# Optimization experiments

Hardware: AMD Instinct MI355X
Metric: run time of the kernel (lower is better)

## Reference

```python
import jax, jax.numpy as jnp
import numpy as np

N_NODES = 50000


def _gcn_conv(h, src, dst, W, b):
    # h: [N, d_in] -> [N, d_out]; symmetric-normalized aggregation with self-loops
    N = h.shape[0]
    h = h @ W  # transform first (d_out < d_in), like PyG GCNConv
    deg = jax.ops.segment_sum(jnp.ones_like(dst, dtype=h.dtype), dst, num_segments=N)
    dinv = jnp.where(deg > 0, jax.lax.rsqrt(jnp.maximum(deg, 1.0)), 0.0)
    norm = dinv[src] * dinv[dst]  # [E']
    msg = h[src] * norm[:, None]  # [E', d_out]
    out = jax.ops.segment_sum(msg, dst, num_segments=N)
    return out + b


def setup_inputs() -> dict:
    key = jax.random.key(0)
    k1, k2, k3, k4 = jax.random.split(key, 4)
    dim_in, dim_h, dim_out, E = 512, 96, 40, 800000
    x = jax.random.normal(k1, (N_NODES, dim_in), dtype=jnp.float32)
    edge_index = jax.random.randint(k2, (2, E), 0, N_NODES, dtype=jnp.int64)
    W1 = jax.random.normal(k3, (dim_in, dim_h), dtype=jnp.float32) / np.sqrt(dim_in)
    b1 = jnp.zeros((dim_h,), dtype=jnp.float32)
    W2 = jax.random.normal(k4, (dim_h, dim_out), dtype=jnp.float32) / np.sqrt(dim_h)
    b2 = jnp.zeros((dim_out,), dtype=jnp.float32)
    return {"x": x, "edge_index": edge_index, "W1": W1, "b1": b1, "W2": W2, "b2": b2}


def reference(x, edge_index, W1, b1, W2, b2):
    N = x.shape[0]
    loops = jnp.arange(N, dtype=edge_index.dtype)
    src = jnp.concatenate([edge_index[0], loops])
    dst = jnp.concatenate([edge_index[1], loops])
    h = jax.nn.relu(_gcn_conv(x, src, dst, W1, b1))
    # dropout p=0.5 is identity in eval mode (training=False)
    logits = _gcn_conv(h, src, dst, W2, b2)
    return (logits, jax.nn.log_softmax(logits, axis=1))
```

## Files before the change

### kernel.cpp

```cpp
#include <hip/hip_runtime.h>
#include <hip/hip_bf16.h>
#include <cstdint>
#include <cstddef>

#define DIN 512
#define DH  96
#define DOUT 40

typedef __attribute__((ext_vector_type(8))) short s8v;
typedef __attribute__((ext_vector_type(4))) float f4v;

__device__ __forceinline__ ushort f2bf(float f) {
    uint u = __float_as_uint(f);
    u += 0x7fffu + ((u >> 16) & 1u);
    return (ushort)(u >> 16);
}
__device__ __forceinline__ uint f2bf2(float lo, float hi) {
    __hip_bfloat162 h = __float22bfloat162_rn(make_float2(lo, hi));
    return *(uint*)&h;
}
__device__ __forceinline__ float bflo(uint u) { return __uint_as_float(u << 16); }
__device__ __forceinline__ float bfhi(uint u) { return __uint_as_float(u & 0xffff0000u); }

__global__ __launch_bounds__(256) void k_prep(
    const float* __restrict__ W1, const float* __restrict__ W2,
    int* __restrict__ cnt, ushort* __restrict__ W1T, ushort* __restrict__ W2T, int N)
{
    int i = blockIdx.x * 256 + threadIdx.x;
    if (i < N) cnt[i] = 0;
    if (i < DIN * DH) {
        int k = i / DH, n = i % DH;
        W1T[(size_t)n * DIN + k] = f2bf(W1[i]);
    }
    if (i < 48 * DH) {
        int n = i / DH, k = i % DH;
        W2T[i] = (n < DOUT) ? f2bf(W2[(size_t)k * DOUT + n]) : (ushort)0;
    }
}

__global__ __launch_bounds__(256) void k_hist(
    const int* __restrict__ dst, int* __restrict__ cnt, int* __restrict__ pos, int E)
{
    int e = blockIdx.x * 256 + threadIdx.x;
    if (e < E) pos[e] = atomicAdd(&cnt[dst[e]], 1);
}

__global__ __launch_bounds__(256) void k_blocksum(const int* __restrict__ cnt, int* __restrict__ bsum, int N) {
    int i = blockIdx.x * 256 + threadIdx.x;
    int c = (i < N) ? cnt[i] : 0;
    #pragma unroll
    for (int off = 32; off >= 1; off >>= 1) c += __shfl_down(c, off, 64);
    __shared__ int wsum[4];
    if ((threadIdx.x & 63) == 0) wsum[threadIdx.x >> 6] = c;
    __syncthreads();
    if (threadIdx.x == 0) bsum[blockIdx.x] = wsum[0] + wsum[1] + wsum[2] + wsum[3];
}

__global__ __launch_bounds__(256) void k_scan_small(const int* __restrict__ bsum, int* __restrict__ boff, int SB) {
    __shared__ int p[256];
    int tid = threadIdx.x;
    int v = (tid < SB) ? bsum[tid] : 0;
    p[tid] = v;
    __syncthreads();
    #pragma unroll
    for (int off = 1; off < 256; off <<= 1) {
        int t = (tid >= off) ? p[tid - off] : 0;
        __syncthreads();
        p[tid] += t;
        __syncthreads();
    }
    if (tid < SB) boff[tid] = p[tid] - v;
}

__global__ __launch_bounds__(256) void k_rowptr(
    const int* __restrict__ cnt, const int* __restrict__ boff,
    int* __restrict__ row_ptr, float* __restrict__ dinv, int N)
{
    __shared__ int p[256];
    int tid = threadIdx.x;
    int i = blockIdx.x * 256 + tid;
    int c = (i < N) ? cnt[i] : 0;
    p[tid] = c;
    __syncthreads();
    #pragma unroll
    for (int off = 1; off < 256; off <<= 1) {
        int t = (tid >= off) ? p[tid - off] : 0;
        __syncthreads();
        p[tid] += t;
        __syncthreads();
    }
    int excl = p[tid] - c;
    if (i < N) {
        int base = boff[blockIdx.x] + excl;
        row_ptr[i] = base;
        dinv[i] = rsqrtf(1.0f + (float)c);
        if (i == N - 1) row_ptr[N] = base + c;
    }
}

__global__ __launch_bounds__(256) void k_fill(
    const int* __restrict__ src, const int* __restrict__ dst,
    const int* __restrict__ row_ptr, const int* __restrict__ pos,
    int* __restrict__ adj, int E)
{
    int e = blockIdx.x * 256 + threadIdx.x;
    if (e >= E) return;
    adj[row_ptr[dst[e]] + pos[e]] = src[e];
}

__global__ __launch_bounds__(256) void k_gemm1(
    const float* __restrict__ x, const ushort* __restrict__ W1T,
    const float* __restrict__ dinv, ushort* __restrict__ hs1, int N)
{
    __shared__ __align__(16) ushort lds[28672];
    const int tid = threadIdx.x;
    const int row0 = blockIdx.x * 128;
    const int lane = tid & 63, w = tid >> 6;
    const int rb = (w >> 1) * 64, cb = (w & 1) * 48;
    const int lm = lane & 15, lq = lane >> 4;

    int aof[4][2], bof[3][2];
    #pragma unroll
    for (int i = 0; i < 4; ++i)
        #pragma unroll
        for (int ks = 0; ks < 2; ++ks) {
            int r = rb + i * 16 + lm, c = ks * 32 + lq * 8;
            aof[i][ks] = r * 64 + (c ^ ((r & 7) << 3));
        }
    #pragma unroll
    for (int j = 0; j < 3; ++j)
        #pragma unroll
        for (int ks = 0; ks < 2; ++ks) {
            int n = cb + j * 16 + lm, c = ks * 32 + lq * 8;
            bof[j][ks] = 16384 + n * 64 + (c ^ ((n & 7) << 3));
        }

    f4v acc[4][3];
    #pragma unroll
    for (int i = 0; i < 4; ++i)
        #pragma unroll
        for (int j = 0; j < 3; ++j) acc[i][j] = (f4v)0.f;

    const int sr = tid >> 1, scb = (tid & 1) * 32;

    auto stage = [&](int kt, int buf) {
        int k0 = kt * 64;
        int gr = row0 + sr;
        ushort* A = lds + buf * 8192;
        #pragma unroll
        for (int s = 0; s < 4; ++s) {
            int c = scb + s * 8;
            float4 v0 = make_float4(0.f, 0.f, 0.f, 0.f), v1 = v0;
            if (gr < N) {
                const float* pp = &x[(size_t)gr * DIN + k0 + c];
                v0 = *(const float4*)pp;
                v1 = *(const float4*)(pp + 4);
            }
            uint4 wv;
            wv.x = f2bf2(v0.x, v0.y);
            wv.y = f2bf2(v0.z, v0.w);
            wv.z = f2bf2(v1.x, v1.y);
            wv.w = f2bf2(v1.z, v1.w);
            *(uint4*)&A[sr * 64 + (c ^ ((sr & 7) << 3))] = wv;
        }
        ushort* B = lds + 16384 + buf * 6144;
        #pragma unroll
        for (int it = 0; it < 3; ++it) {
            int ss = tid + it * 256;
            int n = ss >> 3, c = (ss & 7) * 8;
            uint4 wv = *(const uint4*)&W1T[(size_t)n * DIN + k0 + c];
            *(uint4*)&B[n * 64 + (c ^ ((n & 7) << 3))] = wv;
        }
    };

    stage(0, 0);
    for (int kt = 0; kt < 8; ++kt) {
        __syncthreads();
        if (kt < 7) stage(kt + 1, (kt + 1) & 1);
        const int ab = (kt & 1) * 8192;
        const int bb = (kt & 1) * 6144;
        #pragma unroll
        for (int ks = 0; ks < 2; ++ks) {
            s8v b0 = *(s8v*)&lds[bof[0][ks] + bb];
            s8v b1 = *(s8v*)&lds[bof[1][ks] + bb];
            s8v b2 = *(s8v*)&lds[bof[2][ks] + bb];
            #pragma unroll
            for (int i = 0; i < 4; ++i) {
                s8v a = *(s8v*)&lds[aof[i][ks] + ab];
                acc[i][0] = __builtin_amdgcn_mfma_f32_16x16x32_bf16(a, b0, acc[i][0], 0, 0, 0);
                acc[i][1] = __builtin_amdgcn_mfma_f32_16x16x32_bf16(a, b1, acc[i][1], 0, 0, 0);
                acc[i][2] = __builtin_amdgcn_mfma_f32_16x16x32_bf16(a, b2, acc[i][2], 0, 0, 0);
            }
        }
    }

    #pragma unroll
    for (int i = 0; i < 4; ++i) {
        int gr0 = row0 + rb + i * 16 + lq * 4;
        #pragma unroll
        for (int q = 0; q < 4; ++q) {
            int gr = gr0 + q;
            if (gr < N) {
                float di = dinv[gr];
                #pragma unroll
                for (int j = 0; j < 3; ++j)
                    hs1[(size_t)gr * DH + cb + j * 16 + lm] = f2bf(acc[i][j][q] * di);
            }
        }
    }
}

__global__ __launch_bounds__(256) void k_agg1(
    const int* __restrict__ row_ptr, const int* __restrict__ adj,
    const float* __restrict__ dinv, const ushort* __restrict__ hs1,
    const float* __restrict__ b1, ushort* __restrict__ h1, int N)
{
    int t = blockIdx.x * 256 + threadIdx.x;
    int node = t >> 6, lane = t & 63;
    if (node >= N) return;
    int c = lane << 1;
    const bool act = (c < DH);

    float a0 = 0.f, a1 = 0.f;
    if (act) {
        uint u = *(const uint*)&hs1[(size_t)node * DH + c];
        a0 = bflo(u); a1 = bfhi(u);
    }
    int e = row_ptr[node], e1 = row_ptr[node + 1];
    for (; e + 7 < e1; e += 8) {
        int s0 = adj[e],     s1 = adj[e + 1], s2 = adj[e + 2], s3 = adj[e + 3];
        int s4 = adj[e + 4], s5 = adj[e + 5], s6 = adj[e + 6], s7 = adj[e + 7];
        if (act) {
            uint u0 = *(const uint*)&hs1[(size_t)s0 * DH + c];
            uint u1 = *(const uint*)&hs1[(size_t)s1 * DH + c];
            uint u2 = *(const uint*)&hs1[(size_t)s2 * DH + c];
            uint u3 = *(const uint*)&hs1[(size_t)s3 * DH + c];
            uint u4 = *(const uint*)&hs1[(size_t)s4 * DH + c];
            uint u5 = *(const uint*)&hs1[(size_t)s5 * DH + c];
            uint u6 = *(const uint*)&hs1[(size_t)s6 * DH + c];
            uint u7 = *(const uint*)&hs1[(size_t)s7 * DH + c];
            a0 += bflo(u0); a1 += bfhi(u0);
            a0 += bflo(u1); a1 += bfhi(u1);
            a0 += bflo(u2); a1 += bfhi(u2);
            a0 += bflo(u3); a1 += bfhi(u3);
            a0 += bflo(u4); a1 += bfhi(u4);
            a0 += bflo(u5); a1 += bfhi(u5);
            a0 += bflo(u6); a1 += bfhi(u6);
            a0 += bflo(u7); a1 += bfhi(u7);
        }
    }
    for (; e < e1; ++e) {
        int s = adj[e];
        if (act) {
            uint u = *(const uint*)&hs1[(size_t)s * DH + c];
            a0 += bflo(u); a1 += bfhi(u);
        }
    }
    if (act) {
        float di = dinv[node];
        float r0 = fmaxf(fmaf(a0, di, b1[c]), 0.f);
        float r1 = fmaxf(fmaf(a1, di, b1[c + 1]), 0.f);
        *(uint*)&h1[(size_t)node * DH + c] = f2bf2(r0, r1);
    }
}

__global__ __launch_bounds__(256) void k_gemm2(
    const ushort* __restrict__ h1, const ushort* __restrict__ W2T,
    const float* __restrict__ dinv, float* __restrict__ hs2, int N)
{
    __shared__ __align__(16) ushort lds[16384 + 48 * 128];
    const int tid = threadIdx.x;
    const int row0 = blockIdx.x * 128;

    for (int f = tid; f < 576; f += 256) {
        int r = f / 12, c = (f % 12) * 8;
        uint4 v = *(const uint4*)&W2T[r * DH + c];
        *(uint4*)&lds[16384 + r * 128 + (c ^ ((r & 7) << 3))] = v;
    }
    {
        int r = tid >> 1, half = tid & 1;
        int gr = row0 + r;
        #pragma unroll
        for (int i = 0; i < 6; ++i) {
            int c = half * 48 + i * 8;
            uint4 v = make_uint4(0, 0, 0, 0);
            if (gr < N) v = *(const uint4*)&h1[(size_t)gr * DH + c];
            *(uint4*)&lds[r * 128 + (c ^ ((r & 7) << 3))] = v;
        }
    }
    __syncthreads();

    const int lane = tid & 63, w = tid >> 6;
    const int rb = w * 32, lm = lane & 15, lq = lane >> 4;
    f4v acc[2][3];
    #pragma unroll
    for (int i = 0; i < 2; ++i)
        #pragma unroll
        for (int j = 0; j < 3; ++j) acc[i][j] = (f4v)0.f;

    #pragma unroll
    for (int ks = 0; ks < 3; ++ks) {
        int kk = ks * 32 + lq * 8;
        s8v b[3];
        #pragma unroll
        for (int j = 0; j < 3; ++j) {
            int n = j * 16 + lm;
            b[j] = *(s8v*)&lds[16384 + n * 128 + (kk ^ ((n & 7) << 3))];
        }
        #pragma unroll
        for (int i = 0; i < 2; ++i) {
            int r = rb + i * 16 + lm;
            s8v a = *(s8v*)&lds[r * 128 + (kk ^ ((r & 7) << 3))];
            #pragma unroll
            for (int j = 0; j < 3; ++j)
                acc[i][j] = __builtin_amdgcn_mfma_f32_16x16x32_bf16(a, b[j], acc[i][j], 0, 0, 0);
        }
    }

    #pragma unroll
    for (int i = 0; i < 2; ++i) {
        int gr0 = row0 + rb + i * 16 + lq * 4;
        #pragma unroll
        for (int q = 0; q < 4; ++q) {
            int gr = gr0 + q;
            if (gr < N) {
                float di = dinv[gr];
                #pragma unroll
                for (int j = 0; j < 3; ++j) {
                    int col = j * 16 + lm;
                    if (col < DOUT)
                        hs2[(size_t)gr * DOUT + col] = acc[i][j][q] * di;
                }
            }
        }
    }
}

__global__ __launch_bounds__(256) void k_agg2sm(
    const int* __restrict__ row_ptr, const int* __restrict__ adj,
    const float* __restrict__ dinv, const float* __restrict__ hs2,
    const float* __restrict__ b2, float* __restrict__ out,
    float* __restrict__ lsm, int N)
{
    int t = blockIdx.x * 256 + threadIdx.x;
    int node = t >> 6, lane = t & 63;
    if (node >= N) return;
    const bool act = lane < DOUT;

    float acc = act ? hs2[(size_t)node * DOUT + lane] : 0.f;
    int e = row_ptr[node], e1 = row_ptr[node + 1];
    for (; e + 7 < e1; e += 8) {
        int s0 = adj[e],     s1 = adj[e + 1], s2 = adj[e + 2], s3 = adj[e + 3];
        int s4 = adj[e + 4], s5 = adj[e + 5], s6 = adj[e + 6], s7 = adj[e + 7];
        if (act) {
            float v0 = hs2[(size_t)s0 * DOUT + lane];
            float v1 = hs2[(size_t)s1 * DOUT + lane];
            float v2 = hs2[(size_t)s2 * DOUT + lane];
            float v3 = hs2[(size_t)s3 * DOUT + lane];
            float v4 = hs2[(size_t)s4 * DOUT + lane];
            float v5 = hs2[(size_t)s5 * DOUT + lane];
            float v6 = hs2[(size_t)s6 * DOUT + lane];
            float v7 = hs2[(size_t)s7 * DOUT + lane];
            acc += ((v0 + v1) + (v2 + v3)) + ((v4 + v5) + (v6 + v7));
        }
    }
    for (; e < e1; ++e) {
        int s = adj[e];
        if (act) acc += hs2[(size_t)s * DOUT + lane];
    }

    float v = act ? fmaf(acc, dinv[node], b2[lane]) : -1e30f;
    float m = v;
    #pragma unroll
    for (int off = 32; off >= 1; off >>= 1) m = fmaxf(m, __shfl_xor(m, off));
    float ex = act ? __expf(v - m) : 0.f;
    float s = ex;
    #pragma unroll
    for (int off = 32; off >= 1; off >>= 1) s += __shfl_xor(s, off);
    float lse = m + __logf(s);
    if (act) {
        out[(size_t)node * DOUT + lane] = v;
        lsm[(size_t)node * DOUT + lane] = v - lse;
    }
}

extern "C" void kernel_launch(void* const* d_in, const int* in_sizes, int n_in,
                              void* d_out, int out_size, void* d_ws, size_t ws_size,
                              hipStream_t stream) {
    const float* x  = (const float*)d_in[0];
    const int*   ei = (const int*)d_in[1];
    const float* W1 = (const float*)d_in[2];
    const float* b1 = (const float*)d_in[3];
    const float* W2 = (const float*)d_in[4];
    const float* b2 = (const float*)d_in[5];

    const int N = in_sizes[0] / DIN;
    const int E = in_sizes[1] / 2;
    const int* srcp = ei;
    const int* dstp = ei + E;
    const int SB = (N + 255) / 256;

    ushort* hs1 = (ushort*)d_ws;
    ushort* h1  = hs1 + (size_t)N * DH;
    float* hs2  = (float*)(h1 + (size_t)N * DH);
    float* dinv = hs2 + (size_t)N * DOUT;
    ushort* W1T = (ushort*)(dinv + N);
    ushort* W2T = W1T + (size_t)DH * DIN;
    int* cnt     = (int*)(W2T + 48 * DH);
    int* row_ptr = cnt + N;
    int* adj     = row_ptr + N + 1;
    int* pos     = adj + E;
    int* bsum    = pos + E;
    int* boff    = bsum + SB;

    float* out = (float*)d_out;
    float* lsm = out + (size_t)N * DOUT;

    const int gE = (E + 255) / 256;

    k_prep<<<SB, 256, 0, stream>>>(W1, W2, cnt, W1T, W2T, N);
    k_hist<<<gE, 256, 0, stream>>>(dstp, cnt, pos, E);
    k_blocksum<<<SB, 256, 0, stream>>>(cnt, bsum, N);
    k_scan_small<<<1, 256, 0, stream>>>(bsum, boff, SB);
    k_rowptr<<<SB, 256, 0, stream>>>(cnt, boff, row_ptr, dinv, N);
    k_fill<<<gE, 256, 0, stream>>>(srcp, dstp, row_ptr, pos, adj, E);

    k_gemm1<<<(N + 127) / 128, 256, 0, stream>>>(x, W1T, dinv, hs1, N);
    k_agg1<<<(int)(((size_t)N * 64 + 255) / 256), 256, 0, stream>>>(row_ptr, adj, dinv, hs1, b1, h1, N);

    k_gemm2<<<(N + 127) / 128, 256, 0, stream>>>(h1, W2T, dinv, hs2, N);
    k_agg2sm<<<(int)(((size_t)N * 64 + 255) / 256), 256, 0, stream>>>(row_ptr, adj, dinv, hs2, b2, out, lsm, N);
}
```

Baseline: 185.2 us.

## Store layer-2 features as padded bf16 and shrink gemm1 K-tile

The layer-2 transformed features are now written as bf16 in a 64-wide padded row (128 bytes) instead of fp32 with 40 columns, and the second aggregation reads them two columns per lane. This halves the bytes gathered per edge in the irregular neighbour gather and aligns rows to cache lines. Separately, gemm1 now stages K in 32-wide tiles over 16 iterations with half the LDS and a new swizzle, which may raise occupancy but adds more barriers. It also adds a bf16 rounding of the layer-2 messages, which slightly reduces accuracy.

```diff
diff --git a/kernel.cpp b/kernel.cpp
--- a/kernel.cpp
+++ b/kernel.cpp
@@ -108,48 +108,46 @@
     adj[row_ptr[dst[e]] + pos[e]] = src[e];
 }
 
+#define SWZ(r) (((r >> 1) & 3) << 3)
 __global__ __launch_bounds__(256) void k_gemm1(
     const float* __restrict__ x, const ushort* __restrict__ W1T,
     const float* __restrict__ dinv, ushort* __restrict__ hs1, int N)
 {
-    __shared__ __align__(16) ushort lds[28672];
+    __shared__ __align__(16) ushort lds[14336];
     const int tid = threadIdx.x;
     const int row0 = blockIdx.x * 128;
     const int lane = tid & 63, w = tid >> 6;
     const int rb = (w >> 1) * 64, cb = (w & 1) * 48;
     const int lm = lane & 15, lq = lane >> 4;
 
-    int aof[4][2], bof[3][2];
+    int aof[4], bof[3];
+    #pragma unroll
+    for (int i = 0; i < 4; ++i) {
+        int r = rb + i * 16 + lm;
+        aof[i] = r * 32 + ((lq * 8) ^ SWZ(r));
+    }
+    #pragma unroll
+    for (int j = 0; j < 3; ++j) {
+        int n = cb + j * 16 + lm;
+        bof[j] = 8192 + n * 32 + ((lq * 8) ^ SWZ(n));
+    }
+
+    f4v acc[4][3];
     #pragma unroll
     for (int i = 0; i < 4; ++i)
         #pragma unroll
-        for (int ks = 0; ks < 2; ++ks) {
-            int r = rb + i * 16 + lm, c = ks * 32 + lq * 8;
-            aof[i][ks] = r * 64 + (c ^ ((r & 7) << 3));
-        }
-    #pragma unroll
-    for (int j = 0; j < 3; ++j)
-        #pragma unroll
-        for (int ks = 0; ks < 2; ++ks) {
-            int n = cb + j * 16 + lm, c = ks * 32 + lq * 8;
-            bof[j][ks] = 16384 + n * 64 + (c ^ ((n & 7) << 3));
-        }
-
-    f4v acc[4][3];
-    #pragma unroll
-    for (int i = 0; i < 4; ++i)
-        #pragma unroll
         for (int j = 0; j < 3; ++j) acc[i][j] = (f4v)0.f;
 
-    const int sr = tid >> 1, scb = (tid & 1) * 32;
+    const int sr = tid >> 1;
+    const int c0 = (tid & 1) * 16;
 
     auto stage = [&](int kt, int buf) {
-        int k0 = kt * 64;
+        int k0 = kt * 32;
         int gr = row0 + sr;
-        ushort* A = lds + buf * 8192;
-        #pragma unroll
-        for (int s = 0; s < 4; ++s) {
-            int c = scb + s * 8;
+        ushort* A = lds + buf * 4096;
+        #pragma unroll
+        for (int s = 0; s < 2; ++s) {
+            int c = c0 + s * 8;
             float4 v0 = make_float4(0.f, 0.f, 0.f, 0.f), v1 = v0;
             if (gr < N) {
                 const float* pp = &x[(size_t)gr * DIN + k0 + c];
@@ -161,36 +159,32 @@
             wv.y = f2bf2(v0.z, v0.w);
             wv.z = f2bf2(v1.x, v1.y);
             wv.w = f2bf2(v1.z, v1.w);
-            *(uint4*)&A[sr * 64 + (c ^ ((sr & 7) << 3))] = wv;
-        }
-        ushort* B = lds + 16384 + buf * 6144;
-        #pragma unroll
-        for (int it = 0; it < 3; ++it) {
-            int ss = tid + it * 256;
-            int n = ss >> 3, c = (ss & 7) * 8;
+            *(uint4*)&A[sr * 32 + (c ^ SWZ(sr))] = wv;
+        }
+        ushort* B = lds + 8192 + buf * 3072;
+        #pragma unroll
+        for (int f = tid; f < 384; f += 256) {
+            int n = f >> 2, c = (f & 3) * 8;
             uint4 wv = *(const uint4*)&W1T[(size_t)n * DIN + k0 + c];
-            *(uint4*)&B[n * 64 + (c ^ ((n & 7) << 3))] = wv;
+            *(uint4*)&B[n * 32 + (c ^ SWZ(n))] = wv;
         }
     };
 
     stage(0, 0);
-    for (int kt = 0; kt < 8; ++kt) {
+    for (int kt = 0; kt < 16; ++kt) {
         __syncthreads();
-        if (kt < 7) stage(kt + 1, (kt + 1) & 1);
-        const int ab = (kt & 1) * 8192;
-        const int bb = (kt & 1) * 6144;
-        #pragma unroll
-        for (int ks = 0; ks < 2; ++ks) {
-            s8v b0 = *(s8v*)&lds[bof[0][ks] + bb];
-            s8v b1 = *(s8v*)&lds[bof[1][ks] + bb];
-            s8v b2 = *(s8v*)&lds[bof[2][ks] + bb];
-            #pragma unroll
-            for (int i = 0; i < 4; ++i) {
-                s8v a = *(s8v*)&lds[aof[i][ks] + ab];
-                acc[i][0] = __builtin_amdgcn_mfma_f32_16x16x32_bf16(a, b0, acc[i][0], 0, 0, 0);
-                acc[i][1] = __builtin_amdgcn_mfma_f32_16x16x32_bf16(a, b1, acc[i][1], 0, 0, 0);
-                acc[i][2] = __builtin_amdgcn_mfma_f32_16x16x32_bf16(a, b2, acc[i][2], 0, 0, 0);
-            }
+        if (kt < 15) stage(kt + 1, (kt + 1) & 1);
+        const int ab = (kt & 1) * 4096;
+        const int bb = (kt & 1) * 3072;
+        s8v b0 = *(s8v*)&lds[bof[0] + bb];
+        s8v b1 = *(s8v*)&lds[bof[1] + bb];
+        s8v b2 = *(s8v*)&lds[bof[2] + bb];
+        #pragma unroll
+        for (int i = 0; i < 4; ++i) {
+            s8v a = *(s8v*)&lds[aof[i] + ab];
+            acc[i][0] = __builtin_amdgcn_mfma_f32_16x16x32_bf16(a, b0, acc[i][0], 0, 0, 0);
+            acc[i][1] = __builtin_amdgcn_mfma_f32_16x16x32_bf16(a, b1, acc[i][1], 0, 0, 0);
+            acc[i][2] = __builtin_amdgcn_mfma_f32_16x16x32_bf16(a, b2, acc[i][2], 0, 0, 0);
         }
     }
 
@@ -266,7 +260,7 @@
 
 __global__ __launch_bounds__(256) void k_gemm2(
     const ushort* __restrict__ h1, const ushort* __restrict__ W2T,
-    const float* __restrict__ dinv, float* __restrict__ hs2, int N)
+    const float* __restrict__ dinv, ushort* __restrict__ hs2b, int N)
 {
     __shared__ __align__(16) ushort lds[16384 + 48 * 128];
     const int tid = threadIdx.x;
@@ -329,7 +323,7 @@
                 for (int j = 0; j < 3; ++j) {
                     int col = j * 16 + lm;
                     if (col < DOUT)
-                        hs2[(size_t)gr * DOUT + col] = acc[i][j][q] * di;
+                        hs2b[(size_t)gr * 64 + col] = f2bf(acc[i][j][q] * di);
                 }
             }
         }
@@ -338,49 +332,66 @@
 
 __global__ __launch_bounds__(256) void k_agg2sm(
     const int* __restrict__ row_ptr, const int* __restrict__ adj,
-    const float* __restrict__ dinv, const float* __restrict__ hs2,
+    const float* __restrict__ dinv, const ushort* __restrict__ hs2b,
     const float* __restrict__ b2, float* __restrict__ out,
     float* __restrict__ lsm, int N)
 {
     int t = blockIdx.x * 256 + threadIdx.x;
     int node = t >> 6, lane = t & 63;
     if (node >= N) return;
-    const bool act = lane < DOUT;
-
-    float acc = act ? hs2[(size_t)node * DOUT + lane] : 0.f;
+    int c = lane << 1;
+    const bool act = (c < DOUT);
+
+    float a0 = 0.f, a1 = 0.f;
+    if (act) {
+        uint u = *(const uint*)&hs2b[(size_t)node * 64 + c];
+        a0 = bflo(u); a1 = bfhi(u);
+    }
     int e = row_ptr[node], e1 = row_ptr[node + 1];
     for (; e + 7 < e1; e += 8) {
         int s0 = adj[e],     s1 = adj[e + 1], s2 = adj[e + 2], s3 = adj[e + 3];
         int s4 = adj[e + 4], s5 = adj[e + 5], s6 = adj[e + 6], s7 = adj[e + 7];
         if (act) {
-            float v0 = hs2[(size_t)s0 * DOUT + lane];
-            float v1 = hs2[(size_t)s1 * DOUT + lane];
-            float v2 = hs2[(size_t)s2 * DOUT + lane];
-            float v3 = hs2[(size_t)s3 * DOUT + lane];
-            float v4 = hs2[(size_t)s4 * DOUT + lane];
-            float v5 = hs2[(size_t)s5 * DOUT + lane];
-            float v6 = hs2[(size_t)s6 * DOUT + lane];
-            float v7 = hs2[(size_t)s7 * DOUT + lane];
-            acc += ((v0 + v1) + (v2 + v3)) + ((v4 + v5) + (v6 + v7));
+            uint u0 = *(const uint*)&hs2b[(size_t)s0 * 64 + c];
+            uint u1 = *(const uint*)&hs2b[(size_t)s1 * 64 + c];
+            uint u2 = *(const uint*)&hs2b[(size_t)s2 * 64 + c];
+            uint u3 = *(const uint*)&hs2b[(size_t)s3 * 64 + c];
+            uint u4 = *(const uint*)&hs2b[(size_t)s4 * 64 + c];
+            uint u5 = *(const uint*)&hs2b[(size_t)s5 * 64 + c];
+            uint u6 = *(const uint*)&hs2b[(size_t)s6 * 64 + c];
+            uint u7 = *(const uint*)&hs2b[(size_t)s7 * 64 + c];
+            a0 += bflo(u0); a1 += bfhi(u0);
+            a0 += bflo(u1); a1 += bfhi(u1);
+            a0 += bflo(u2); a1 += bfhi(u2);
+            a0 += bflo(u3); a1 += bfhi(u3);
+            a0 += bflo(u4); a1 += bfhi(u4);
+            a0 += bflo(u5); a1 += bfhi(u5);
+            a0 += bflo(u6); a1 += bfhi(u6);
+            a0 += bflo(u7); a1 += bfhi(u7);
         }
     }
     for (; e < e1; ++e) {
         int s = adj[e];
-        if (act) acc += hs2[(size_t)s * DOUT + lane];
-    }
-
-    float v = act ? fmaf(acc, dinv[node], b2[lane]) : -1e30f;
-    float m = v;
+        if (act) {
+            uint u = *(const uint*)&hs2b[(size_t)s * 64 + c];
+            a0 += bflo(u); a1 += bfhi(u);
+        }
+    }
+
+    float di = act ? dinv[node] : 0.f;
+    float v0 = act ? fmaf(a0, di, b2[c]) : -1e30f;
+    float v1 = act ? fmaf(a1, di, b2[c + 1]) : -1e30f;
+    float m = fmaxf(v0, v1);
     #pragma unroll
     for (int off = 32; off >= 1; off >>= 1) m = fmaxf(m, __shfl_xor(m, off));
-    float ex = act ? __expf(v - m) : 0.f;
+    float ex = act ? (__expf(v0 - m) + __expf(v1 - m)) : 0.f;
     float s = ex;
     #pragma unroll
     for (int off = 32; off >= 1; off >>= 1) s += __shfl_xor(s, off);
     float lse = m + __logf(s);
     if (act) {
-        out[(size_t)node * DOUT + lane] = v;
-        lsm[(size_t)node * DOUT + lane] = v - lse;
+        *(float2*)&out[(size_t)node * DOUT + c] = make_float2(v0, v1);
+        *(float2*)&lsm[(size_t)node * DOUT + c] = make_float2(v0 - lse, v1 - lse);
     }
 }
 
@@ -400,12 +411,12 @@
     const int* dstp = ei + E;
     const int SB = (N + 255) / 256;
 
-    ushort* hs1 = (ushort*)d_ws;
-    ushort* h1  = hs1 + (size_t)N * DH;
-    float* hs2  = (float*)(h1 + (size_t)N * DH);
-    float* dinv = hs2 + (size_t)N * DOUT;
-    ushort* W1T = (ushort*)(dinv + N);
-    ushort* W2T = W1T + (size_t)DH * DIN;
+    ushort* hs1  = (ushort*)d_ws;
+    ushort* h1   = hs1 + (size_t)N * DH;
+    ushort* hs2b = h1 + (size_t)N * DH;
+    float* dinv  = (float*)(hs2b + (size_t)N * 64);
+    ushort* W1T  = (ushort*)(dinv + N);
+    ushort* W2T  = W1T + (size_t)DH * DIN;
     int* cnt     = (int*)(W2T + 48 * DH);
     int* row_ptr = cnt + N;
     int* adj     = row_ptr + N + 1;
@@ -428,6 +439,6 @@
     k_gemm1<<<(N + 127) / 128, 256, 0, stream>>>(x, W1T, dinv, hs1, N);
     k_agg1<<<(int)(((size_t)N * 64 + 255) / 256), 256, 0, stream>>>(row_ptr, adj, dinv, hs1, b1, h1, N);
 
-    k_gemm2<<<(N + 127) / 128, 256, 0, stream>>>(h1, W2T, dinv, hs2, N);
-    k_agg2sm<<<(int)(((size_t)N * 64 + 255) / 256), 256, 0, stream>>>(row_ptr, adj, dinv, hs2, b2, out, lsm, N);
-}
+    k_gemm2<<<(N + 127) / 128, 256, 0, stream>>>(h1, W2T, dinv, hs2b, N);
+    k_agg2sm<<<(int)(((size_t)N * 64 + 255) / 256), 256, 0, stream>>>(row_ptr, adj, dinv, hs2b, b2, out, lsm, N);
+}
```

New measurement: 181.3 us. 2.1% less time.
